# Kernel optimization log

Measured on AMD Instinct MI355X. Metric: run time of the kernel, lower is better.

The kernel has to match this reference:

```python
import jax, jax.numpy as jnp
import numpy as np

EPS = 1e-5
B, HD, LD, OD, E = 4, 256, 512, 256, 64  # E = out_dim // reduction
H, W, H2, W2 = 64, 64, 32, 32

def conv1x1(x, Wt, b=None):
    # x: [B,C,H,W], Wt: [O,C]
    y = jnp.einsum('bchw,oc->bohw', x, Wt)
    if b is not None:
        y = y + b[None, :, None, None]
    return y

def bn(x, s, bi, m, v):
    # eval-mode BatchNorm2d with running stats
    inv = (s / jnp.sqrt(v + EPS))[None, :, None, None]
    return (x - m[None, :, None, None]) * inv + bi[None, :, None, None]

def setup_inputs() -> dict:
    key = jax.random.key(0)
    ks = jax.random.split(key, 24)
    def n(k, shape, scale=0.05):
        return jax.random.normal(k, shape, dtype=jnp.float32) * scale
    inp = {
        'high_feat': jax.random.normal(ks[0], (B, HD, H, W), dtype=jnp.float32),
        'low_feat': jax.random.normal(ks[1], (B, LD, H2, W2), dtype=jnp.float32),
        'W_high': n(ks[2], (E, HD)),
        'bn_h_scale': 1.0 + n(ks[3], (E,)), 'bn_h_bias': n(ks[4], (E,)),
        'bn_h_mean': n(ks[5], (E,)), 'bn_h_var': 0.5 + jax.random.uniform(ks[6], (E,), dtype=jnp.float32),
        'W_low': n(ks[7], (E, LD)),
        'bn_l_scale': 1.0 + n(ks[8], (E,)), 'bn_l_bias': n(ks[9], (E,)),
        'bn_l_mean': n(ks[10], (E,)), 'bn_l_var': 0.5 + jax.random.uniform(ks[11], (E,), dtype=jnp.float32),
        'W_q': n(ks[12], (E, E)), 'b_q': n(ks[13], (E,)),
        'W_k': n(ks[14], (E, E)), 'b_k': n(ks[15], (E,)),
        'W_vh': n(ks[16], (OD, HD)), 'b_vh': n(ks[17], (OD,)),
        'W_vl': n(ks[18], (OD, LD)), 'b_vl': n(ks[19], (OD,)),
        'W_out': n(ks[20], (OD, 2 * OD)),
        'bn_o_scale': 1.0 + n(ks[21], (OD,)), 'bn_o_bias': n(ks[22], (OD,)),
        'bn_o_mean': jnp.zeros((OD,), jnp.float32), 'bn_o_var': jnp.ones((OD,), jnp.float32),
        'gamma': n(ks[23], (1,), scale=0.5),
    }
    return inp

def reference(high_feat, low_feat, W_high, bn_h_scale, bn_h_bias, bn_h_mean, bn_h_var,
              W_low, bn_l_scale, bn_l_bias, bn_l_mean, bn_l_var,
              W_q, b_q, W_k, b_k, W_vh, b_vh, W_vl, b_vl,
              W_out, bn_o_scale, bn_o_bias, bn_o_mean, bn_o_var, gamma):
    N = H * W
    # bilinear upsample low_feat to high_feat spatial size (align_corners=False)
    low = jax.image.resize(low_feat, (B, LD, H, W), method='bilinear')
    he = jax.nn.relu(bn(conv1x1(high_feat, W_high), bn_h_scale, bn_h_bias, bn_h_mean, bn_h_var))
    le = jax.nn.relu(bn(conv1x1(low, W_low), bn_l_scale, bn_l_bias, bn_l_mean, bn_l_var))
    q = conv1x1(he, W_q, b_q).reshape(B, E, N)   # [B,E,N1]
    k = conv1x1(le, W_k, b_k).reshape(B, E, N)   # [B,E,N2]
    energy = jnp.einsum('bcn,bcm->bnm', q, k)    # [B,N1,N2]
    attn = jax.nn.softmax(energy, axis=-1)
    vh = conv1x1(high_feat, W_vh, b_vh).reshape(B, OD, N)
    vl = conv1x1(low, W_vl, b_vl).reshape(B, OD, N)
    out_high = jnp.einsum('bcm,bnm->bcn', vh, attn).reshape(B, OD, H, W)
    out_low = jnp.einsum('bcn,bnm->bcm', vl, attn).reshape(B, OD, H, W)
    cat = jnp.concatenate([out_high, out_low], axis=1)  # [B,2*OD,H,W]
    out = jax.nn.relu(bn(conv1x1(cat, W_out), bn_o_scale, bn_o_bias, bn_o_mean, bn_o_var))
    return high_feat + gamma[0] * out
```

## Files before the change

### kernel.cpp

```cpp
#include <hip/hip_runtime.h>
#include <hip/hip_bf16.h>

#define B_   4
#define HD_  256
#define LD_  512
#define OD_  256
#define E_   64
#define N_   4096
#define N2_  1024
#define EPS_ 1e-5f

typedef __hip_bfloat16 bf16;
typedef __attribute__((ext_vector_type(8))) short short8;
typedef __attribute__((ext_vector_type(4))) float floatx4;

#define MFMA16(a, b, c) __builtin_amdgcn_mfma_f32_16x16x32_bf16(a, b, c, 0, 0, 0)

#define GLOAD(dst, ptr) \
  asm volatile("global_load_dwordx4 %0, %1, off" : "=v"(dst) : "v"(ptr) : "memory")
#define VWAIT() do { \
  asm volatile("s_waitcnt vmcnt(0)" ::: "memory"); \
  __builtin_amdgcn_sched_barrier(0); \
} while (0)
#define CVTPK(d, lo, hi) \
  asm("v_cvt_pk_bf16_f32 %0, %1, %2" : "=v"(d) : "v"(lo), "v"(hi))

#define WH_OFF   0
#define WL_OFF   16384
#define WQ_OFF   49152
#define WK_OFF   53248
#define WVH_OFF  57344
#define WVL_OFF  122880
#define WO_OFF   253952
#define WTOT     385024

__device__ __forceinline__ unsigned short f2b_bits(float f) {
  union { float f; unsigned int u; } cv; cv.f = f;
  unsigned int u = cv.u;
  return (unsigned short)((u + 0x7FFFu + ((u >> 16) & 1u)) >> 16);
}
__device__ __forceinline__ float bits2f(unsigned short h) {
  union { unsigned int u; float f; } cv; cv.u = ((unsigned int)h) << 16;
  return cv.f;
}
__device__ __forceinline__ float ldext(const void* p, size_t i, int fl) {
  if (fl) return __bfloat162float(((const bf16*)p)[i]);
  return ((const float*)p)[i];
}
__device__ __forceinline__ short8 ld8(const short* p) { return *(const short8*)p; }
__device__ __forceinline__ short8 i4s8(int4 v) {
  union { int4 i; short8 s; } u; u.i = v; return u.s;
}
__device__ __forceinline__ short8 ldP(const unsigned short* p) {
  return *(const short8*)p;
}

__device__ __forceinline__ size_t frag_off(int r, int k, int K) {
  return ((size_t)(r >> 4) * ((size_t)K << 4)) + ((size_t)(k >> 5) << 9)
       + ((r & 15) << 5) + (k & 31);
}
__device__ __forceinline__ size_t v_off(int c, int m) {
  return ((size_t)(m >> 5) << 13) + ((c >> 4) << 9) + (((m >> 3) & 3) << 7)
       + ((c & 15) << 3) + (m & 7);
}

__global__ void detect_dtype_k(const void* probe, int* dflag) {
  if (threadIdx.x == 0 && blockIdx.x == 0) {
    const unsigned int* u = (const unsigned int*)probe;
    int bf = 1;
    for (int i = 0; i < 32; i++)
      if (u[i] != 0x3F803F80u) bf = 0;
    dflag[0] = bf;
  }
}

__global__ __launch_bounds__(256) void cvt_weights_k(
    const void* Wh, const void* Wl, const void* Wq, const void* Wk,
    const void* Wvh, const void* Wvl, const void* Wo,
    unsigned short* wbuf, const int* dflag)
{
  const int fl = dflag[0];
  int i = blockIdx.x * 256 + threadIdx.x;
  if (i >= WTOT) return;
  const void* src; int li, off, ksh;
  if      (i < WL_OFF)  { src = Wh;  li = i - WH_OFF;  off = WH_OFF;  ksh = 8; }
  else if (i < WQ_OFF)  { src = Wl;  li = i - WL_OFF;  off = WL_OFF;  ksh = 9; }
  else if (i < WK_OFF)  { src = Wq;  li = i - WQ_OFF;  off = WQ_OFF;  ksh = 6; }
  else if (i < WVH_OFF) { src = Wk;  li = i - WK_OFF;  off = WK_OFF;  ksh = 6; }
  else if (i < WVL_OFF) { src = Wvh; li = i - WVH_OFF; off = WVH_OFF; ksh = 8; }
  else if (i < WO_OFF)  { src = Wvl; li = i - WVL_OFF; off = WVL_OFF; ksh = 9; }
  else                  { src = Wo;  li = i - WO_OFF;  off = WO_OFF;  ksh = 9; }
  int K = 1 << ksh;
  int r = li >> ksh, k = li & (K - 1);
  wbuf[off + frag_off(r, k, K)] = f2b_bits(ldext(src, li, fl));
}

__global__ __launch_bounds__(256) void transpose_cvt_k(
    const void* X, unsigned short* Xt, int C, int S, const int* dflag)
{
  __shared__ unsigned short T[64][66];
  const int fl = dflag[0];
  const int tid = threadIdx.x;
  const int s0 = blockIdx.x * 64, c0 = blockIdx.y * 64, b = blockIdx.z;
  const size_t ibase = (size_t)b * C * S;
  const size_t obase = (size_t)b * S * C;
  const int sl = tid & 63, q = tid >> 6;
  for (int i = 0; i < 16; i++) {
    int c = q + i * 4;
    T[c][sl] = f2b_bits(ldext(X, ibase + (size_t)(c0 + c) * S + s0 + sl, fl));
  }
  __syncthreads();
  for (int i = 0; i < 16; i++) {
    int s = q + i * 4;
    Xt[obase + frag_off(s0 + s, c0 + sl, C)] = T[sl][s];
  }
}

__global__ __launch_bounds__(256) void gemm_k(
    const unsigned short* A, long sA,
    const unsigned short* Bm, long sB,
    unsigned short* D, long sD, int ldd,
    int K, int mode, int axis, int swz,
    const void* p0, const void* p1, const void* p2, const void* p3,
    const int* dflag)
{
  const int fl = dflag[0];
  const int tid = threadIdx.x;
  const int w = tid >> 6, lane = tid & 63;
  const int g = lane >> 4, c16 = lane & 15;
  const int r0 = blockIdx.x * 64 + (w >> 1) * 32;
  const int c0 = blockIdx.y * 64 + (w & 1) * 32;
  const short* Ab = (const short*)A + (size_t)blockIdx.z * sA;
  const short* Bb = (const short*)Bm + (size_t)blockIdx.z * sB;
  unsigned short* Db = D + (size_t)blockIdx.z * sD;

  floatx4 acc[2][2];
  #pragma unroll
  for (int i = 0; i < 2; i++)
    #pragma unroll
    for (int j = 0; j < 2; j++) acc[i][j] = (floatx4){0.f, 0.f, 0.f, 0.f};

  for (int k0 = 0; k0 < K; k0 += 64) {
    short8 Af[2][2], Bf[2][2];
    #pragma unroll
    for (int t = 0; t < 2; t++)
      #pragma unroll
      for (int kc = 0; kc < 2; kc++) {
        Af[t][kc] = ld8(Ab + frag_off(r0 + t * 16 + c16, k0 + kc * 32 + g * 8, K));
        Bf[t][kc] = ld8(Bb + frag_off(c0 + t * 16 + c16, k0 + kc * 32 + g * 8, K));
      }
    #pragma unroll
    for (int kc = 0; kc < 2; kc++)
      #pragma unroll
      for (int rt = 0; rt < 2; rt++)
        #pragma unroll
        for (int ct = 0; ct < 2; ct++)
          acc[rt][ct] = MFMA16(Af[rt][kc], Bf[ct][kc], acc[rt][ct]);
  }

  #pragma unroll
  for (int rt = 0; rt < 2; rt++)
    #pragma unroll
    for (int ct = 0; ct < 2; ct++)
      #pragma unroll
      for (int r = 0; r < 4; r++) {
        int rr = r0 + rt * 16 + g * 4 + r;
        int cc = c0 + ct * 16 + c16;
        int pi = axis ? rr : cc;
        float v = acc[rt][ct][r];
        if (mode == 1) v += ldext(p0, pi, fl);
        else if (mode >= 2) {
          float inv = ldext(p0, pi, fl) * rsqrtf(ldext(p3, pi, fl) + EPS_);
          v = v * inv + (ldext(p1, pi, fl) - ldext(p2, pi, fl) * inv);
          if (mode == 3) v = fmaxf(v, 0.f);
        }
        size_t idx;
        if (swz == 1)      idx = frag_off(rr, cc, ldd);
        else if (swz == 2) idx = v_off(rr, cc);
        else               idx = (size_t)rr * ldd + cc;
        Db[idx] = f2b_bits(v);
      }
}

__global__ __launch_bounds__(256) void upsample_rows_k(
    const unsigned short* src, unsigned short* dst, int relu)
{
  int idx = blockIdx.x * 256 + threadIdx.x;
  int e0 = (idx & 7) * 8, n = (idx >> 3) & (N_ - 1), b = idx >> 15;
  int y = n >> 6, x = n & 63;
  int y0 = (y - 1) >> 1;  float wy = (y & 1) ? 0.25f : 0.75f;
  int x0 = (x - 1) >> 1;  float wx = (x & 1) ? 0.25f : 0.75f;
  int y0c = max(y0, 0), y1c = min(y0 + 1, 31);
  int x0c = max(x0, 0), x1c = min(x0 + 1, 31);
  const unsigned short* sb = src + ((size_t)b * N2_) * 64 + e0;
  short8 a00 = ld8((const short*)(sb + (y0c * 32 + x0c) * 64));
  short8 a01 = ld8((const short*)(sb + (y0c * 32 + x1c) * 64));
  short8 a10 = ld8((const short*)(sb + (y1c * 32 + x0c) * 64));
  short8 a11 = ld8((const short*)(sb + (y1c * 32 + x1c) * 64));
  short8 o;
  #pragma unroll
  for (int i = 0; i < 8; i++) {
    float v = (1.f - wy) * ((1.f - wx) * bits2f((unsigned short)a00[i])
                          + wx * bits2f((unsigned short)a01[i]))
            + wy * ((1.f - wx) * bits2f((unsigned short)a10[i])
                          + wx * bits2f((unsigned short)a11[i]));
    if (relu) v = fmaxf(v, 0.f);
    o[i] = (short)f2b_bits(v);
  }
  *(short8*)(dst + (size_t)b * N_ * 64 + frag_off(n, e0, 64)) = o;
}

__global__ __launch_bounds__(256) void upsample_swz_k(
    const unsigned short* src, unsigned short* dst)
{
  int idx = blockIdx.x * 256 + threadIdx.x;
  int n8 = idx & 511, c = (idx >> 9) & 255, b = idx >> 17;
  int n0 = n8 * 8;
  int y = n0 >> 6, xb = n0 & 63;
  int y0 = (y - 1) >> 1;  float wy = (y & 1) ? 0.25f : 0.75f;
  int y0c = max(y0, 0), y1c = min(y0 + 1, 31);
  const unsigned short* sb = src + (size_t)(b * 256 + c) * N2_;
  int sbase = (xb >> 1) - 1;
  float r0[6], r1[6];
  #pragma unroll
  for (int t = 0; t < 6; t++) {
    int xc = min(max(sbase + t, 0), 31);
    r0[t] = bits2f(sb[y0c * 32 + xc]);
    r1[t] = bits2f(sb[y1c * 32 + xc]);
  }
  short8 o;
  #pragma unroll
  for (int j = 0; j < 8; j++) {
    int t = (j + 1) >> 1;
    float wx = (j & 1) ? 0.25f : 0.75f;
    float v = (1.f - wy) * ((1.f - wx) * r0[t] + wx * r0[t + 1])
            + wy * ((1.f - wx) * r1[t] + wx * r1[t + 1]);
    o[j] = (short)f2b_bits(v);
  }
  *(short8*)(dst + (size_t)b * 256 * N_ + v_off(c, n0)) = o;
}


__global__ __launch_bounds__(256, 2) void attn_apply_high_mfma_k(
    const bf16* qt, const bf16* kt, const bf16* vh,
    float* lsum_p, unsigned short* ohp0, unsigned short* ohp1)
{
  __shared__ __align__(16) unsigned short Pb[2][64][136];
  __shared__ float Lw[4][64];
  const int tid = threadIdx.x;
  const int w = tid >> 6, lane = tid & 63;
  const int g = lane >> 4, c16 = lane & 15;
  const int L = blockIdx.x;
  const int b = (L & 7) >> 1;
  const int n0 = (L >> 3) * 64;
  const int half = L & 1;
  const int mbase = half * 2048, mend = mbase + 2048;
  const short* q = (const short*)qt + (size_t)b * N_ * E_;
  const short* k = (const short*)kt + (size_t)b * N_ * E_;
  const short* v = (const short*)vh + (size_t)b * OD_ * N_;

  short8 Bq[4][2];
  #pragma unroll
  for (int nt = 0; nt < 4; nt++)
    #pragma unroll
    for (int ks = 0; ks < 2; ks++)
      Bq[nt][ks] = ld8(q + frag_off(n0 + nt * 16 + c16, ks * 32 + g * 8, 64));

  float lsum[4] = {0.f, 0.f, 0.f, 0.f};
  floatx4 oacc[4][4];
  #pragma unroll
  for (int nt = 0; nt < 4; nt++)
    #pragma unroll
    for (int ct = 0; ct < 4; ct++)
      oacc[nt][ct] = (floatx4){0.f, 0.f, 0.f, 0.f};

  short8 Ak[2][2];
  #pragma unroll
  for (int mt = 0; mt < 2; mt++)
    #pragma unroll
    for (int ks = 0; ks < 2; ks++)
      Ak[mt][ks] = ld8(k + frag_off(mbase + w * 32 + mt * 16 + c16, ks * 32 + g * 8, 64));

  int buf = 0;
  for (int m0 = mbase; m0 < mend; m0 += 128, buf ^= 1) {
    int4 bv[16];
    #pragma unroll
    for (int ks = 0; ks < 4; ks++)
      #pragma unroll
      for (int ct = 0; ct < 4; ct++)
        GLOAD(bv[ks * 4 + ct],
              (v + v_off(w * 64 + ct * 16 + c16, m0 + ks * 32 + g * 8)));
    floatx4 s[2][4];
    #pragma unroll
    for (int mt = 0; mt < 2; mt++)
      #pragma unroll
      for (int nt = 0; nt < 4; nt++) {
        floatx4 z = (floatx4){0.f, 0.f, 0.f, 0.f};
        z = MFMA16(Ak[mt][0], Bq[nt][0], z);
        z = MFMA16(Ak[mt][1], Bq[nt][1], z);
        s[mt][nt] = z;
      }
    int mn_ = m0 + 128;
    if (mn_ < mend) {
      #pragma unroll
      for (int mt = 0; mt < 2; mt++)
        #pragma unroll
        for (int ks = 0; ks < 2; ks++)
          Ak[mt][ks] = ld8(k + frag_off(mn_ + w * 32 + mt * 16 + c16, ks * 32 + g * 8, 64));
    }
    #pragma unroll
    for (int mt = 0; mt < 2; mt++)
      #pragma unroll
      for (int nt = 0; nt < 4; nt++) {
        float p0v = __expf(fminf(s[mt][nt][0], 60.f));
        float p1v = __expf(fminf(s[mt][nt][1], 60.f));
        float p2v = __expf(fminf(s[mt][nt][2], 60.f));
        float p3v = __expf(fminf(s[mt][nt][3], 60.f));
        lsum[nt] += (p0v + p1v) + (p2v + p3v);
        unsigned int d0, d1;
        CVTPK(d0, p0v, p1v);
        CVTPK(d1, p2v, p3v);
        uint2 pk; pk.x = d0; pk.y = d1;
        *(uint2*)&Pb[buf][nt * 16 + c16][w * 32 + mt * 16 + 4 * g] = pk;
      }
    __syncthreads();
    VWAIT();
    #pragma unroll
    for (int ks = 0; ks < 4; ks++) {
      short8 Ap0 = ldP(&Pb[buf][c16][ks * 32 + g * 8]);
      short8 Ap1 = ldP(&Pb[buf][16 + c16][ks * 32 + g * 8]);
      short8 Ap2 = ldP(&Pb[buf][32 + c16][ks * 32 + g * 8]);
      short8 Ap3 = ldP(&Pb[buf][48 + c16][ks * 32 + g * 8]);
      #pragma unroll
      for (int ct = 0; ct < 4; ct++) {
        short8 Bv = i4s8(bv[ks * 4 + ct]);
        oacc[0][ct] = MFMA16(Ap0, Bv, oacc[0][ct]);
        oacc[1][ct] = MFMA16(Ap1, Bv, oacc[1][ct]);
        oacc[2][ct] = MFMA16(Ap2, Bv, oacc[2][ct]);
        oacc[3][ct] = MFMA16(Ap3, Bv, oacc[3][ct]);
      }
    }
  }
  #pragma unroll
  for (int nt = 0; nt < 4; nt++) {
    lsum[nt] += __shfl_xor(lsum[nt], 16);
    lsum[nt] += __shfl_xor(lsum[nt], 32);
  }
  if (g == 0)
    #pragma unroll
    for (int nt = 0; nt < 4; nt++)
      Lw[w][nt * 16 + c16] = lsum[nt];
  __syncthreads();
  if (tid < 64)
    lsum_p[(size_t)half * 16384 + (size_t)b * N_ + n0 + tid] =
        Lw[0][tid] + Lw[1][tid] + Lw[2][tid] + Lw[3][tid];
  unsigned short* op = (half ? ohp1 : ohp0) + (size_t)b * N_ * OD_;
  #pragma unroll
  for (int nt = 0; nt < 4; nt++)
    #pragma unroll
    for (int ct = 0; ct < 4; ct++)
      #pragma unroll
      for (int r = 0; r < 4; r++) {
        int n = n0 + nt * 16 + g * 4 + r;
        int c = w * 64 + ct * 16 + c16;
        op[frag_off(n, c, 256)] = f2b_bits(oacc[nt][ct][r]);
      }
}

__global__ __launch_bounds__(256) void reduce_high_k(
    const unsigned short* p0, const unsigned short* p1, const float* lsum_p,
    unsigned short* oh, float* rsumG)
{
  size_t i8 = ((size_t)blockIdx.x * 256 + threadIdx.x) * 8;
  int slab = (int)(i8 >> 20);
  int loc  = (int)(i8 & 0xFFFFF);
  int n = (loc >> 12) * 16 + ((loc >> 5) & 15);
  int row = slab * N_ + n;
  float l = lsum_p[row] + lsum_p[16384 + row];
  float ri = 1.0f / l;
  const unsigned short* a = p0 + i8;
  const unsigned short* b = p1 + i8;
  short8 o;
  #pragma unroll
  for (int i = 0; i < 8; i++)
    o[i] = (short)f2b_bits((bits2f(a[i]) + bits2f(b[i])) * ri);
  *(short8*)(oh + i8) = o;
  if ((loc & 31) == 0) rsumG[row] = ri;
}

__global__ __launch_bounds__(256, 2) void attn_apply_low_mfma_k(
    const bf16* qt, const bf16* kt, const bf16* vl, const float* rinvG,
    unsigned short* olp0, unsigned short* olp1)
{
  __shared__ __align__(16) unsigned short Pb[2][64][136];
  const int tid = threadIdx.x;
  const int w = tid >> 6, lane = tid & 63;
  const int g = lane >> 4, c16 = lane & 15;
  const int L = blockIdx.x;
  const int b = (L & 7) >> 1;
  const int m0 = (L >> 3) * 64;
  const int half = L & 1;
  const int nbase = half * 2048, nend = nbase + 2048;
  const short* q = (const short*)qt + (size_t)b * N_ * E_;
  const short* k = (const short*)kt + (size_t)b * N_ * E_;
  const short* v = (const short*)vl + (size_t)b * OD_ * N_;
  const float* rinv = rinvG + (size_t)b * N_;

  short8 Bk[4][2];
  #pragma unroll
  for (int mt = 0; mt < 4; mt++)
    #pragma unroll
    for (int ks = 0; ks < 2; ks++)
      Bk[mt][ks] = ld8(k + frag_off(m0 + mt * 16 + c16, ks * 32 + g * 8, 64));

  floatx4 oacc[4][4];
  #pragma unroll
  for (int mt = 0; mt < 4; mt++)
    #pragma unroll
    for (int ct = 0; ct < 4; ct++)
      oacc[mt][ct] = (floatx4){0.f, 0.f, 0.f, 0.f};

  short8 Aq[2][2];
  #pragma unroll
  for (int nt = 0; nt < 2; nt++)
    #pragma unroll
    for (int ks = 0; ks < 2; ks++)
      Aq[nt][ks] = ld8(q + frag_off(nbase + w * 32 + nt * 16 + c16, ks * 32 + g * 8, 64));

  int buf = 0;
  for (int nL = nbase; nL < nend; nL += 128, buf ^= 1) {
    int4 bv[16];
    #pragma unroll
    for (int ks = 0; ks < 4; ks++)
      #pragma unroll
      for (int ct = 0; ct < 4; ct++)
        GLOAD(bv[ks * 4 + ct],
              (v + v_off(w * 64 + ct * 16 + c16, nL + ks * 32 + g * 8)));
    floatx4 s[2][4];
    #pragma unroll
    for (int nt = 0; nt < 2; nt++)
      #pragma unroll
      for (int mt = 0; mt < 4; mt++) {
        floatx4 z = (floatx4){0.f, 0.f, 0.f, 0.f};
        z = MFMA16(Aq[nt][0], Bk[mt][0], z);
        z = MFMA16(Aq[nt][1], Bk[mt][1], z);
        s[nt][mt] = z;
      }
    int nn_ = nL + 128;
    if (nn_ < nend) {
      #pragma unroll
      for (int nt = 0; nt < 2; nt++)
        #pragma unroll
        for (int ks = 0; ks < 2; ks++)
          Aq[nt][ks] = ld8(q + frag_off(nn_ + w * 32 + nt * 16 + c16, ks * 32 + g * 8, 64));
    }
    #pragma unroll
    for (int nt = 0; nt < 2; nt++) {
      const float4 rv = *(const float4*)(rinv + nL + w * 32 + nt * 16 + 4 * g);
      #pragma unroll
      for (int mt = 0; mt < 4; mt++) {
        float p0v = __expf(fminf(s[nt][mt][0], 60.f)) * rv.x;
        float p1v = __expf(fminf(s[nt][mt][1], 60.f)) * rv.y;
        float p2v = __expf(fminf(s[nt][mt][2], 60.f)) * rv.z;
        float p3v = __expf(fminf(s[nt][mt][3], 60.f)) * rv.w;
        unsigned int d0, d1;
        CVTPK(d0, p0v, p1v);
        CVTPK(d1, p2v, p3v);
        uint2 pk; pk.x = d0; pk.y = d1;
        *(uint2*)&Pb[buf][mt * 16 + c16][w * 32 + nt * 16 + 4 * g] = pk;
      }
    }
    __syncthreads();
    VWAIT();
    #pragma unroll
    for (int ks = 0; ks < 4; ks++) {
      short8 Ap0 = ldP(&Pb[buf][c16][ks * 32 + g * 8]);
      short8 Ap1 = ldP(&Pb[buf][16 + c16][ks * 32 + g * 8]);
      short8 Ap2 = ldP(&Pb[buf][32 + c16][ks * 32 + g * 8]);
      short8 Ap3 = ldP(&Pb[buf][48 + c16][ks * 32 + g * 8]);
      #pragma unroll
      for (int ct = 0; ct < 4; ct++) {
        short8 Bv = i4s8(bv[ks * 4 + ct]);
        oacc[0][ct] = MFMA16(Ap0, Bv, oacc[0][ct]);
        oacc[1][ct] = MFMA16(Ap1, Bv, oacc[1][ct]);
        oacc[2][ct] = MFMA16(Ap2, Bv, oacc[2][ct]);
        oacc[3][ct] = MFMA16(Ap3, Bv, oacc[3][ct]);
      }
    }
  }
  unsigned short* op = (half ? olp1 : olp0) + (size_t)b * N_ * OD_;
  #pragma unroll
  for (int mt = 0; mt < 4; mt++)
    #pragma unroll
    for (int ct = 0; ct < 4; ct++)
      #pragma unroll
      for (int r = 0; r < 4; r++) {
        int m = m0 + mt * 16 + g * 4 + r;
        int c = w * 64 + ct * 16 + c16;
        op[frag_off(m, c, 256)] = f2b_bits(oacc[mt][ct][r]);
      }
}

__global__ __launch_bounds__(256) void reduce_low_k(
    const unsigned short* p0, const unsigned short* p1, unsigned short* ol)
{
  size_t i8 = ((size_t)blockIdx.x * 256 + threadIdx.x) * 8;
  const unsigned short* a = p0 + i8;
  const unsigned short* b = p1 + i8;
  short8 o;
  #pragma unroll
  for (int i = 0; i < 8; i++)
    o[i] = (short)f2b_bits(bits2f(a[i]) + bits2f(b[i]));
  *(short8*)(ol + i8) = o;
}

__global__ __launch_bounds__(256) void final_mfma_k(
    const unsigned short* Wo, const unsigned short* oh, const unsigned short* ol,
    const void* sc, const void* bi, const void* mn, const void* vr,
    const void* hf, const void* gamma, void* out, const int* dflag)
{
  const int fl = dflag[0];
  const int tid = threadIdx.x;
  const int w = tid >> 6, lane = tid & 63;
  const int g = lane >> 4, c16 = lane & 15;
  const int r0 = blockIdx.x * 64 + (w >> 1) * 32;
  const int c0 = blockIdx.y * 64 + (w & 1) * 32;
  const int b = blockIdx.z;

  floatx4 acc[2][2];
  #pragma unroll
  for (int i = 0; i < 2; i++)
    #pragma unroll
    for (int j = 0; j < 2; j++) acc[i][j] = (floatx4){0.f, 0.f, 0.f, 0.f};

  #pragma unroll
  for (int half = 0; half < 2; half++) {
    const short* Bb = (const short*)(half ? ol : oh) + (size_t)b * N_ * 256;
    for (int k0 = 0; k0 < 256; k0 += 64) {
      short8 Af[2][2], Bf[2][2];
      #pragma unroll
      for (int t = 0; t < 2; t++)
        #pragma unroll
        for (int kc = 0; kc < 2; kc++) {
          Af[t][kc] = ld8((const short*)Wo + frag_off(r0 + t * 16 + c16,
                          half * 256 + k0 + kc * 32 + g * 8, 512));
          Bf[t][kc] = ld8(Bb + frag_off(c0 + t * 16 + c16, k0 + kc * 32 + g * 8, 256));
        }
      #pragma unroll
      for (int kc = 0; kc < 2; kc++)
        #pragma unroll
        for (int rt = 0; rt < 2; rt++)
          #pragma unroll
          for (int ct = 0; ct < 2; ct++)
            acc[rt][ct] = MFMA16(Af[rt][kc], Bf[ct][kc], acc[rt][ct]);
    }
  }

  float gm = ldext(gamma, 0, fl);
  #pragma unroll
  for (int rt = 0; rt < 2; rt++)
    #pragma unroll
    for (int r = 0; r < 4; r++) {
      int o = r0 + rt * 16 + g * 4 + r;
      float inv = ldext(sc, o, fl) * rsqrtf(ldext(vr, o, fl) + EPS_);
      float bb = ldext(bi, o, fl) - ldext(mn, o, fl) * inv;
      #pragma unroll
      for (int ct = 0; ct < 2; ct++) {
        int n = c0 + ct * 16 + c16;
        float v = acc[rt][ct][r] * inv + bb;
        v = fmaxf(v, 0.f);
        size_t idx = ((size_t)b * OD_ + o) * N_ + n;
        float res = ldext(hf, idx, fl) + gm * v;
        if (fl) ((bf16*)out)[idx] = __float2bfloat16(res);
        else    ((float*)out)[idx] = res;
      }
    }
}

extern "C" void kernel_launch(void* const* d_in, const int* in_sizes, int n_in,
                              void* d_out, int out_size, void* d_ws, size_t ws_size,
                              hipStream_t stream)
{
  const void* hf     = d_in[0];
  const void* lf     = d_in[1];
  const void* W_high = d_in[2];
  const void* bhs = d_in[3],  *bhb = d_in[4],  *bhm = d_in[5],  *bhv = d_in[6];
  const void* W_low  = d_in[7];
  const void* bls = d_in[8],  *blb = d_in[9],  *blm = d_in[10], *blv = d_in[11];
  const void* W_q    = d_in[12], *b_q = d_in[13];
  const void* W_k    = d_in[14], *b_k = d_in[15];
  const void* W_vh   = d_in[16], *b_vh = d_in[17];
  const void* W_vl   = d_in[18], *b_vl = d_in[19];
  const void* W_out  = d_in[20];
  const void* bos = d_in[21], *bob = d_in[22], *bom = d_in[23], *bov = d_in[24];
  const void* gamma  = d_in[25];

  char* wp = (char*)d_ws;
  int*   dflag  = (int*)wp;                                 wp += 64;
  float* rsum   = (float*)wp;                               wp += 16384 * 4;
  float* lsum_p = (float*)wp;                               wp += 2 * 16384 * 4;
  unsigned short* wbuf  = (unsigned short*)wp;              wp += WTOT * 2;
  unsigned short* hf_t  = (unsigned short*)wp;              wp += (size_t)B_ * N_ * 256 * 2;
  unsigned short* lf_t  = (unsigned short*)wp;              wp += (size_t)B_ * N2_ * 512 * 2;
  unsigned short* he_t  = (unsigned short*)wp;              wp += (size_t)B_ * N_ * 64 * 2;
  unsigned short* le_sm = (unsigned short*)wp;              wp += (size_t)B_ * N2_ * 64 * 2;
  unsigned short* le_t  = (unsigned short*)wp;              wp += (size_t)B_ * N_ * 64 * 2;
  unsigned short* vl_sm = (unsigned short*)wp;              wp += (size_t)B_ * 256 * N2_ * 2;
  unsigned short* vh    = (unsigned short*)wp;              wp += (size_t)B_ * 256 * N_ * 2;
  unsigned short* vl    = (unsigned short*)wp;              wp += (size_t)B_ * 256 * N_ * 2;
  unsigned short* ol    = (unsigned short*)wp;              wp += (size_t)B_ * N_ * 256 * 2;
  unsigned short* pext  = (unsigned short*)wp;              wp += (size_t)B_ * N_ * 256 * 2;
  unsigned short* oh = hf_t;
  unsigned short* qv = lf_t;
  unsigned short* kv = lf_t + (size_t)B_ * N_ * 64;
  unsigned short* ohp0 = ol;
  unsigned short* ohp1 = pext;
  unsigned short* olp0 = vh;
  unsigned short* olp1 = pext;

  dim3 blk(256);
  detect_dtype_k<<<1, 64, 0, stream>>>(bov, dflag);
  cvt_weights_k<<<(WTOT + 255) / 256, blk, 0, stream>>>(W_high, W_low, W_q, W_k, W_vh, W_vl,
                                                        W_out, wbuf, dflag);
  transpose_cvt_k<<<dim3(64, 4, B_), blk, 0, stream>>>(hf, hf_t, 256, N_, dflag);
  transpose_cvt_k<<<dim3(16, 8, B_), blk, 0, stream>>>(lf, lf_t, 512, N2_, dflag);

  gemm_k<<<dim3(256, 1, 1), blk, 0, stream>>>(hf_t, 0, wbuf + WH_OFF, 0,
      he_t, 0, 64, 256, 3, 0, 1, bhs, bhb, bhm, bhv, dflag);
  gemm_k<<<dim3(4, 64, B_), blk, 0, stream>>>(wbuf + WVH_OFF, 0,
      hf_t, (long)N_ * 256, vh, (long)256 * N_, N_, 256, 1, 1, 2,
      b_vh, b_vh, b_vh, b_vh, dflag);
  gemm_k<<<dim3(64, 1, 1), blk, 0, stream>>>(lf_t, 0, wbuf + WL_OFF, 0,
      le_sm, 0, 64, 512, 2, 0, 0, bls, blb, blm, blv, dflag);
  gemm_k<<<dim3(4, 16, B_), blk, 0, stream>>>(wbuf + WVL_OFF, 0,
      lf_t, (long)N2_ * 512, vl_sm, (long)256 * N2_, N2_, 512, 1, 1, 0,
      b_vl, b_vl, b_vl, b_vl, dflag);
  upsample_rows_k<<<(B_ * N_ * 8) / 256, blk, 0, stream>>>(le_sm, le_t, 1);
  upsample_swz_k <<<(B_ * 256 * 512) / 256, blk, 0, stream>>>(vl_sm, vl);
  gemm_k<<<dim3(256, 1, 1), blk, 0, stream>>>(he_t, 0, wbuf + WQ_OFF, 0,
      qv, 0, 64, 64, 1, 0, 1, b_q, b_q, b_q, b_q, dflag);
  gemm_k<<<dim3(256, 1, 1), blk, 0, stream>>>(le_t, 0, wbuf + WK_OFF, 0,
      kv, 0, 64, 64, 1, 0, 1, b_k, b_k, b_k, b_k, dflag);

  attn_apply_high_mfma_k<<<dim3(512), blk, 0, stream>>>((const bf16*)qv, (const bf16*)kv,
      (const bf16*)vh, lsum_p, ohp0, ohp1);
  reduce_high_k<<<dim3(2048), blk, 0, stream>>>(ohp0, ohp1, lsum_p, oh, rsum);
  attn_apply_low_mfma_k <<<dim3(512), blk, 0, stream>>>((const bf16*)qv, (const bf16*)kv,
      (const bf16*)vl, rsum, olp0, olp1);
  reduce_low_k<<<dim3(2048), blk, 0, stream>>>(olp0, olp1, ol);

  final_mfma_k<<<dim3(4, 64, B_), blk, 0, stream>>>(wbuf + WO_OFF, oh, ol,
      bos, bob, bom, bov, hf, gamma, d_out, dflag);
}
```

Measured before the change: 328.1 us.

## Replace split-K attention halves with 512-thread blocks and drop reduce kernels

Each attention-apply block now covers the full key/query range with 8 waves instead of two 256-thread blocks over halves, so the partial outputs no longer need to be written out and summed. Normalization by the row sum is folded into the high kernel's epilogue, and the separate reduce_high and reduce_low kernels are removed. This cuts two launches and the bf16 partial-buffer round trips. The cost is half as many blocks (256 across the GPU's CUs), larger blocks limited to one per CU, and each wave computing fewer output channels per score tile, which lowers MFMA reuse.

Measured after the change: 340.4 us. 3.8% more time.

```diff
diff --git a/kernel.cpp b/kernel.cpp
--- a/kernel.cpp
+++ b/kernel.cpp
@@ -241,20 +241,19 @@
 }
 
 
-__global__ __launch_bounds__(256, 2) void attn_apply_high_mfma_k(
+__global__ __launch_bounds__(512, 1) void attn_apply_high_mfma_k(
     const bf16* qt, const bf16* kt, const bf16* vh,
-    float* lsum_p, unsigned short* ohp0, unsigned short* ohp1)
+    float* rinvG, unsigned short* oh)
 {
   __shared__ __align__(16) unsigned short Pb[2][64][136];
-  __shared__ float Lw[4][64];
+  __shared__ float Lw[8][64];
+  __shared__ float Ln[64];
   const int tid = threadIdx.x;
   const int w = tid >> 6, lane = tid & 63;
   const int g = lane >> 4, c16 = lane & 15;
   const int L = blockIdx.x;
-  const int b = (L & 7) >> 1;
-  const int n0 = (L >> 3) * 64;
-  const int half = L & 1;
-  const int mbase = half * 2048, mend = mbase + 2048;
+  const int b = L >> 6;
+  const int n0 = (L & 63) * 64;
   const short* q = (const short*)qt + (size_t)b * N_ * E_;
   const short* k = (const short*)kt + (size_t)b * N_ * E_;
   const short* v = (const short*)vh + (size_t)b * OD_ * N_;
@@ -267,62 +266,54 @@
       Bq[nt][ks] = ld8(q + frag_off(n0 + nt * 16 + c16, ks * 32 + g * 8, 64));
 
   float lsum[4] = {0.f, 0.f, 0.f, 0.f};
-  floatx4 oacc[4][4];
+  floatx4 oacc[4][2];
   #pragma unroll
   for (int nt = 0; nt < 4; nt++)
     #pragma unroll
-    for (int ct = 0; ct < 4; ct++)
+    for (int ct = 0; ct < 2; ct++)
       oacc[nt][ct] = (floatx4){0.f, 0.f, 0.f, 0.f};
 
-  short8 Ak[2][2];
-  #pragma unroll
-  for (int mt = 0; mt < 2; mt++)
-    #pragma unroll
-    for (int ks = 0; ks < 2; ks++)
-      Ak[mt][ks] = ld8(k + frag_off(mbase + w * 32 + mt * 16 + c16, ks * 32 + g * 8, 64));
+  short8 Ak[2];
+  #pragma unroll
+  for (int ks = 0; ks < 2; ks++)
+    Ak[ks] = ld8(k + frag_off(w * 16 + c16, ks * 32 + g * 8, 64));
 
   int buf = 0;
-  for (int m0 = mbase; m0 < mend; m0 += 128, buf ^= 1) {
-    int4 bv[16];
+  for (int m0 = 0; m0 < N_; m0 += 128, buf ^= 1) {
+    int4 bv[8];
     #pragma unroll
     for (int ks = 0; ks < 4; ks++)
       #pragma unroll
-      for (int ct = 0; ct < 4; ct++)
-        GLOAD(bv[ks * 4 + ct],
-              (v + v_off(w * 64 + ct * 16 + c16, m0 + ks * 32 + g * 8)));
-    floatx4 s[2][4];
-    #pragma unroll
-    for (int mt = 0; mt < 2; mt++)
-      #pragma unroll
-      for (int nt = 0; nt < 4; nt++) {
-        floatx4 z = (floatx4){0.f, 0.f, 0.f, 0.f};
-        z = MFMA16(Ak[mt][0], Bq[nt][0], z);
-        z = MFMA16(Ak[mt][1], Bq[nt][1], z);
-        s[mt][nt] = z;
-      }
+      for (int ct = 0; ct < 2; ct++)
+        GLOAD(bv[ks * 2 + ct],
+              (v + v_off(w * 32 + ct * 16 + c16, m0 + ks * 32 + g * 8)));
+    floatx4 s[4];
+    #pragma unroll
+    for (int nt = 0; nt < 4; nt++) {
+      floatx4 z = (floatx4){0.f, 0.f, 0.f, 0.f};
+      z = MFMA16(Ak[0], Bq[nt][0], z);
+      z = MFMA16(Ak[1], Bq[nt][1], z);
+      s[nt] = z;
+    }
     int mn_ = m0 + 128;
-    if (mn_ < mend) {
-      #pragma unroll
-      for (int mt = 0; mt < 2; mt++)
-        #pragma unroll
-        for (int ks = 0; ks < 2; ks++)
-          Ak[mt][ks] = ld8(k + frag_off(mn_ + w * 32 + mt * 16 + c16, ks * 32 + g * 8, 64));
-    }
-    #pragma unroll
-    for (int mt = 0; mt < 2; mt++)
-      #pragma unroll
-      for (int nt = 0; nt < 4; nt++) {
-        float p0v = __expf(fminf(s[mt][nt][0], 60.f));
-        float p1v = __expf(fminf(s[mt][nt][1], 60.f));
-        float p2v = __expf(fminf(s[mt][nt][2], 60.f));
-        float p3v = __expf(fminf(s[mt][nt][3], 60.f));
-        lsum[nt] += (p0v + p1v) + (p2v + p3v);
-        unsigned int d0, d1;
-        CVTPK(d0, p0v, p1v);
-        CVTPK(d1, p2v, p3v);
-        uint2 pk; pk.x = d0; pk.y = d1;
-        *(uint2*)&Pb[buf][nt * 16 + c16][w * 32 + mt * 16 + 4 * g] = pk;
-      }
+    if (mn_ < N_) {
+      #pragma unroll
+      for (int ks = 0; ks < 2; ks++)
+        Ak[ks] = ld8(k + frag_off(mn_ + w * 16 + c16, ks * 32 + g * 8, 64));
+    }
+    #pragma unroll
+    for (int nt = 0; nt < 4; nt++) {
+      float p0v = __expf(fminf(s[nt][0], 60.f));
+      float p1v = __expf(fminf(s[nt][1], 60.f));
+      float p2v = __expf(fminf(s[nt][2], 60.f));
+      float p3v = __expf(fminf(s[nt][3], 60.f));
+      lsum[nt] += (p0v + p1v) + (p2v + p3v);
+      unsigned int d0, d1;
+      CVTPK(d0, p0v, p1v);
+      CVTPK(d1, p2v, p3v);
+      uint2 pk; pk.x = d0; pk.y = d1;
+      *(uint2*)&Pb[buf][nt * 16 + c16][w * 16 + 4 * g] = pk;
+    }
     __syncthreads();
     VWAIT();
     #pragma unroll
@@ -332,8 +323,8 @@
       short8 Ap2 = ldP(&Pb[buf][32 + c16][ks * 32 + g * 8]);
       short8 Ap3 = ldP(&Pb[buf][48 + c16][ks * 32 + g * 8]);
       #pragma unroll
-      for (int ct = 0; ct < 4; ct++) {
-        short8 Bv = i4s8(bv[ks * 4 + ct]);
+      for (int ct = 0; ct < 2; ct++) {
+        short8 Bv = i4s8(bv[ks * 2 + ct]);
         oacc[0][ct] = MFMA16(Ap0, Bv, oacc[0][ct]);
         oacc[1][ct] = MFMA16(Ap1, Bv, oacc[1][ct]);
         oacc[2][ct] = MFMA16(Ap2, Bv, oacc[2][ct]);
@@ -351,56 +342,40 @@
     for (int nt = 0; nt < 4; nt++)
       Lw[w][nt * 16 + c16] = lsum[nt];
   __syncthreads();
-  if (tid < 64)
-    lsum_p[(size_t)half * 16384 + (size_t)b * N_ + n0 + tid] =
-        Lw[0][tid] + Lw[1][tid] + Lw[2][tid] + Lw[3][tid];
-  unsigned short* op = (half ? ohp1 : ohp0) + (size_t)b * N_ * OD_;
+  if (tid < 64) {
+    float l = (Lw[0][tid] + Lw[1][tid]) + (Lw[2][tid] + Lw[3][tid])
+            + (Lw[4][tid] + Lw[5][tid]) + (Lw[6][tid] + Lw[7][tid]);
+    float ri = 1.0f / l;
+    Ln[tid] = ri;
+    rinvG[(size_t)b * N_ + n0 + tid] = ri;
+  }
+  __syncthreads();
+  unsigned short* op = oh + (size_t)b * N_ * OD_;
   #pragma unroll
   for (int nt = 0; nt < 4; nt++)
     #pragma unroll
-    for (int ct = 0; ct < 4; ct++)
-      #pragma unroll
-      for (int r = 0; r < 4; r++) {
-        int n = n0 + nt * 16 + g * 4 + r;
-        int c = w * 64 + ct * 16 + c16;
-        op[frag_off(n, c, 256)] = f2b_bits(oacc[nt][ct][r]);
+    for (int r = 0; r < 4; r++) {
+      float ri = Ln[nt * 16 + g * 4 + r];
+      int n = n0 + nt * 16 + g * 4 + r;
+      #pragma unroll
+      for (int ct = 0; ct < 2; ct++) {
+        int c = w * 32 + ct * 16 + c16;
+        op[frag_off(n, c, 256)] = f2b_bits(oacc[nt][ct][r] * ri);
       }
-}
-
-__global__ __launch_bounds__(256) void reduce_high_k(
-    const unsigned short* p0, const unsigned short* p1, const float* lsum_p,
-    unsigned short* oh, float* rsumG)
-{
-  size_t i8 = ((size_t)blockIdx.x * 256 + threadIdx.x) * 8;
-  int slab = (int)(i8 >> 20);
-  int loc  = (int)(i8 & 0xFFFFF);
-  int n = (loc >> 12) * 16 + ((loc >> 5) & 15);
-  int row = slab * N_ + n;
-  float l = lsum_p[row] + lsum_p[16384 + row];
-  float ri = 1.0f / l;
-  const unsigned short* a = p0 + i8;
-  const unsigned short* b = p1 + i8;
-  short8 o;
-  #pragma unroll
-  for (int i = 0; i < 8; i++)
-    o[i] = (short)f2b_bits((bits2f(a[i]) + bits2f(b[i])) * ri);
-  *(short8*)(oh + i8) = o;
-  if ((loc & 31) == 0) rsumG[row] = ri;
-}
-
-__global__ __launch_bounds__(256, 2) void attn_apply_low_mfma_k(
+    }
+}
+
+__global__ __launch_bounds__(512, 1) void attn_apply_low_mfma_k(
     const bf16* qt, const bf16* kt, const bf16* vl, const float* rinvG,
-    unsigned short* olp0, unsigned short* olp1)
+    unsigned short* ol)
 {
   __shared__ __align__(16) unsigned short Pb[2][64][136];
   const int tid = threadIdx.x;
   const int w = tid >> 6, lane = tid & 63;
   const int g = lane >> 4, c16 = lane & 15;
   const int L = blockIdx.x;
-  const int b = (L & 7) >> 1;
-  const int m0 = (L >> 3) * 64;
-  const int half = L & 1;
-  const int nbase = half * 2048, nend = nbase + 2048;
+  const int b = L >> 6;
+  const int m0 = (L & 63) * 64;
   const short* q = (const short*)qt + (size_t)b * N_ * E_;
   const short* k = (const short*)kt + (size_t)b * N_ * E_;
   const short* v = (const short*)vl + (size_t)b * OD_ * N_;
@@ -413,62 +388,53 @@
     for (int ks = 0; ks < 2; ks++)
       Bk[mt][ks] = ld8(k + frag_off(m0 + mt * 16 + c16, ks * 32 + g * 8, 64));
 
-  floatx4 oacc[4][4];
+  floatx4 oacc[4][2];
   #pragma unroll
   for (int mt = 0; mt < 4; mt++)
     #pragma unroll
-    for (int ct = 0; ct < 4; ct++)
+    for (int ct = 0; ct < 2; ct++)
       oacc[mt][ct] = (floatx4){0.f, 0.f, 0.f, 0.f};
 
-  short8 Aq[2][2];
-  #pragma unroll
-  for (int nt = 0; nt < 2; nt++)
-    #pragma unroll
-    for (int ks = 0; ks < 2; ks++)
-      Aq[nt][ks] = ld8(q + frag_off(nbase + w * 32 + nt * 16 + c16, ks * 32 + g * 8, 64));
+  short8 Aq[2];
+  #pragma unroll
+  for (int ks = 0; ks < 2; ks++)
+    Aq[ks] = ld8(q + frag_off(w * 16 + c16, ks * 32 + g * 8, 64));
 
   int buf = 0;
-  for (int nL = nbase; nL < nend; nL += 128, buf ^= 1) {
-    int4 bv[16];
+  for (int nL = 0; nL < N_; nL += 128, buf ^= 1) {
+    int4 bv[8];
     #pragma unroll
     for (int ks = 0; ks < 4; ks++)
       #pragma unroll
-      for (int ct = 0; ct < 4; ct++)
-        GLOAD(bv[ks * 4 + ct],
-              (v + v_off(w * 64 + ct * 16 + c16, nL + ks * 32 + g * 8)));
-    floatx4 s[2][4];
-    #pragma unroll
-    for (int nt = 0; nt < 2; nt++)
-      #pragma unroll
-      for (int mt = 0; mt < 4; mt++) {
-        floatx4 z = (floatx4){0.f, 0.f, 0.f, 0.f};
-        z = MFMA16(Aq[nt][0], Bk[mt][0], z);
-        z = MFMA16(Aq[nt][1], Bk[mt][1], z);
-        s[nt][mt] = z;
-      }
+      for (int ct = 0; ct < 2; ct++)
+        GLOAD(bv[ks * 2 + ct],
+              (v + v_off(w * 32 + ct * 16 + c16, nL + ks * 32 + g * 8)));
+    floatx4 s[4];
+    #pragma unroll
+    for (int mt = 0; mt < 4; mt++) {
+      floatx4 z = (floatx4){0.f, 0.f, 0.f, 0.f};
+      z = MFMA16(Aq[0], Bk[mt][0], z);
+      z = MFMA16(Aq[1], Bk[mt][1], z);
+      s[mt] = z;
+    }
     int nn_ = nL + 128;
-    if (nn_ < nend) {
-      #pragma unroll
-      for (int nt = 0; nt < 2; nt++)
-        #pragma unroll
-        for (int ks = 0; ks < 2; ks++)
-          Aq[nt][ks] = ld8(q + frag_off(nn_ + w * 32 + nt * 16 + c16, ks * 32 + g * 8, 64));
-    }
-    #pragma unroll
-    for (int nt = 0; nt < 2; nt++) {
-      const float4 rv = *(const float4*)(rinv + nL + w * 32 + nt * 16 + 4 * g);
-      #pragma unroll
-      for (int mt = 0; mt < 4; mt++) {
-        float p0v = __expf(fminf(s[nt][mt][0], 60.f)) * rv.x;
-        float p1v = __expf(fminf(s[nt][mt][1], 60.f)) * rv.y;
-        float p2v = __expf(fminf(s[nt][mt][2], 60.f)) * rv.z;
-        float p3v = __expf(fminf(s[nt][mt][3], 60.f)) * rv.w;
-        unsigned int d0, d1;
-        CVTPK(d0, p0v, p1v);
-        CVTPK(d1, p2v, p3v);
-        uint2 pk; pk.x = d0; pk.y = d1;
-        *(uint2*)&Pb[buf][mt * 16 + c16][w * 32 + nt * 16 + 4 * g] = pk;
-      }
+    if (nn_ < N_) {
+      #pragma unroll
+      for (int ks = 0; ks < 2; ks++)
+        Aq[ks] = ld8(q + frag_off(nn_ + w * 16 + c16, ks * 32 + g * 8, 64));
+    }
+    const float4 rv = *(const float4*)(rinv + nL + w * 16 + 4 * g);
+    #pragma unroll
+    for (int mt = 0; mt < 4; mt++) {
+      float p0v = __expf(fminf(s[mt][0], 60.f)) * rv.x;
+      float p1v = __expf(fminf(s[mt][1], 60.f)) * rv.y;
+      float p2v = __expf(fminf(s[mt][2], 60.f)) * rv.z;
+      float p3v = __expf(fminf(s[mt][3], 60.f)) * rv.w;
+      unsigned int d0, d1;
+      CVTPK(d0, p0v, p1v);
+      CVTPK(d1, p2v, p3v);
+      uint2 pk; pk.x = d0; pk.y = d1;
+      *(uint2*)&Pb[buf][mt * 16 + c16][w * 16 + 4 * g] = pk;
     }
     __syncthreads();
     VWAIT();
@@ -479,8 +445,8 @@
       short8 Ap2 = ldP(&Pb[buf][32 + c16][ks * 32 + g * 8]);
       short8 Ap3 = ldP(&Pb[buf][48 + c16][ks * 32 + g * 8]);
       #pragma unroll
-      for (int ct = 0; ct < 4; ct++) {
-        short8 Bv = i4s8(bv[ks * 4 + ct]);
+      for (int ct = 0; ct < 2; ct++) {
+        short8 Bv = i4s8(bv[ks * 2 + ct]);
         oacc[0][ct] = MFMA16(Ap0, Bv, oacc[0][ct]);
         oacc[1][ct] = MFMA16(Ap1, Bv, oacc[1][ct]);
         oacc[2][ct] = MFMA16(Ap2, Bv, oacc[2][ct]);
@@ -488,30 +454,17 @@
       }
     }
   }
-  unsigned short* op = (half ? olp1 : olp0) + (size_t)b * N_ * OD_;
+  unsigned short* op = ol + (size_t)b * N_ * OD_;
   #pragma unroll
   for (int mt = 0; mt < 4; mt++)
     #pragma unroll
-    for (int ct = 0; ct < 4; ct++)
+    for (int ct = 0; ct < 2; ct++)
       #pragma unroll
       for (int r = 0; r < 4; r++) {
         int m = m0 + mt * 16 + g * 4 + r;
-        int c = w * 64 + ct * 16 + c16;
+        int c = w * 32 + ct * 16 + c16;
         op[frag_off(m, c, 256)] = f2b_bits(oacc[mt][ct][r]);
       }
-}
-
-__global__ __launch_bounds__(256) void reduce_low_k(
-    const unsigned short* p0, const unsigned short* p1, unsigned short* ol)
-{
-  size_t i8 = ((size_t)blockIdx.x * 256 + threadIdx.x) * 8;
-  const unsigned short* a = p0 + i8;
-  const unsigned short* b = p1 + i8;
-  short8 o;
-  #pragma unroll
-  for (int i = 0; i < 8; i++)
-    o[i] = (short)f2b_bits(bits2f(a[i]) + bits2f(b[i]));
-  *(short8*)(ol + i8) = o;
 }
 
 __global__ __launch_bounds__(256) void final_mfma_k(
@@ -611,14 +564,13 @@
   unsigned short* ol    = (unsigned short*)wp;              wp += (size_t)B_ * N_ * 256 * 2;
   unsigned short* pext  = (unsigned short*)wp;              wp += (size_t)B_ * N_ * 256 * 2;
   unsigned short* oh = hf_t;
+
   unsigned short* qv = lf_t;
   unsigned short* kv = lf_t + (size_t)B_ * N_ * 64;
-  unsigned short* ohp0 = ol;
-  unsigned short* ohp1 = pext;
-  unsigned short* olp0 = vh;
-  unsigned short* olp1 = pext;
+  (void)lsum_p; (void)pext;
 
   dim3 blk(256);
+  dim3 blk512(512);
   detect_dtype_k<<<1, 64, 0, stream>>>(bov, dflag);
   cvt_weights_k<<<(WTOT + 255) / 256, blk, 0, stream>>>(W_high, W_low, W_q, W_k, W_vh, W_vl,
                                                         W_out, wbuf, dflag);
@@ -642,12 +594,10 @@
   gemm_k<<<dim3(256, 1, 1), blk, 0, stream>>>(le_t, 0, wbuf + WK_OFF, 0,
       kv, 0, 64, 64, 1, 0, 1, b_k, b_k, b_k, b_k, dflag);
 
-  attn_apply_high_mfma_k<<<dim3(512), blk, 0, stream>>>((const bf16*)qv, (const bf16*)kv,
-      (const bf16*)vh, lsum_p, ohp0, ohp1);
-  reduce_high_k<<<dim3(2048), blk, 0, stream>>>(ohp0, ohp1, lsum_p, oh, rsum);
-  attn_apply_low_mfma_k <<<dim3(512), blk, 0, stream>>>((const bf16*)qv, (const bf16*)kv,
-      (const bf16*)vl, rsum, olp0, olp1);
-  reduce_low_k<<<dim3(2048), blk, 0, stream>>>(olp0, olp1, ol);
+  attn_apply_high_mfma_k<<<dim3(256), blk512, 0, stream>>>((const bf16*)qv, (const bf16*)kv,
+      (const bf16*)vh, rsum, oh);
+  attn_apply_low_mfma_k <<<dim3(256), blk512, 0, stream>>>((const bf16*)qv, (const bf16*)kv,
+      (const bf16*)vl, rsum, ol);
 
   final_mfma_k<<<dim3(4, 64, B_), blk, 0, stream>>>(wbuf + WO_OFF, oh, ol,
       bos, bob, bom, bov, hf, gamma, d_out, dflag);
```
